# Optimization experiments

Measured on AMD Instinct MI355X. Metric: run time of the kernel, lower is better.

Reference implementation:

```python
import jax, jax.numpy as jnp
import numpy as np

B, S, E, H = 4, 1024, 1024, 16
D = E // H  # head_dim = 64


def setup_inputs() -> dict:
    key = jax.random.key(0)
    ks = jax.random.split(key, 12)
    s = 1.0 / np.sqrt(E)
    return {
        "query": jax.random.normal(ks[0], (B, S, E), jnp.float32),
        "key_": jax.random.normal(ks[1], (B, S, E), jnp.float32),
        "value": jax.random.normal(ks[2], (B, S, E), jnp.float32),
        "mask": jnp.ones((B, S, S), dtype=bool),
        "Wq": jax.random.uniform(ks[3], (E, E), jnp.float32, -s, s),
        "bq": jax.random.uniform(ks[4], (E,), jnp.float32, -s, s),
        "Wk": jax.random.uniform(ks[5], (E, E), jnp.float32, -s, s),
        "bk": jax.random.uniform(ks[6], (E,), jnp.float32, -s, s),
        "Wv": jax.random.uniform(ks[7], (E, E), jnp.float32, -s, s),
        "bv": jax.random.uniform(ks[8], (E,), jnp.float32, -s, s),
        "Wo": jax.random.uniform(ks[9], (E, E), jnp.float32, -s, s),
        "bo": jax.random.uniform(ks[10], (E,), jnp.float32, -s, s),
    }


def reference(query, key_, value, mask, Wq, bq, Wk, bk, Wv, bv, Wo, bo):
    # project and split heads: [B,S,E] -> [B,H,S,D]
    def heads(x, W, b):
        return (x @ W + b).reshape(B, -1, H, D).transpose(0, 2, 1, 3)

    q = heads(query, Wq, bq)
    k = heads(key_, Wk, bk)
    v = heads(value, Wv, bv)

    scores = jnp.einsum("bhqd,bhkd->bhqk", q, k) / jnp.sqrt(jnp.float32(D))
    # bool mask: positions where mask==0 are filled with -1e9
    scores = jnp.where(mask[:, None, :, :], scores, jnp.float32(-1e9))
    attn_weights = jax.nn.softmax(scores, axis=-1)  # [B,H,Sq,Sk]
    out = jnp.einsum("bhqk,bhkd->bhqd", attn_weights, v)
    out = out.transpose(0, 2, 1, 3).reshape(B, -1, E)  # [B,Sq,E]
    attn_output = out @ Wo + bo
    return attn_output, attn_weights
```

## Files before the change

kernel.cpp:

```cpp
#include <hip/hip_runtime.h>
#include <stdint.h>

typedef __bf16 bf16;
typedef bf16 bf16x2 __attribute__((ext_vector_type(2)));
typedef bf16 bf16x4 __attribute__((ext_vector_type(4)));
typedef bf16 bf16x8 __attribute__((ext_vector_type(8)));
typedef float f32x4 __attribute__((ext_vector_type(4)));
typedef float f32x16 __attribute__((ext_vector_type(16)));

static constexpr int Bc = 4, Sc = 1024, Ec = 1024, Hc = 16, Dc = 64, BSc = 4096;

__device__ __forceinline__ void gld_lds16(const void* g, void* s) {
  __builtin_amdgcn_global_load_lds((const __attribute__((address_space(1))) void*)g,
                                   (__attribute__((address_space(3))) void*)s, 16, 0, 0);
}

__global__ void detect_mask_kernel(const uint8_t* __restrict__ mask, int* flag) {
  if (threadIdx.x == 0 && blockIdx.x == 0) {
    bool everyGroupHasZero = true;
    bool anyNonzero = false;
    for (int j = 0; j < 16; ++j) {
      bool z = false;
      for (int bjj = 0; bjj < 4; ++bjj) {
        uint8_t byte = mask[4 * j + bjj];
        if (byte == 0) z = true;
        if (byte != 0) anyNonzero = true;
      }
      if (!z) everyGroupHasZero = false;
    }
    flag[0] = (everyGroupHasZero && anyNonzero) ? 4 : 1;
    flag[1] = 1;
  }
}

__global__ __launch_bounds__(256) void prep_kernel(
    const float* __restrict__ q, const float* __restrict__ k, const float* __restrict__ v,
    bf16* __restrict__ xb, const uint8_t* __restrict__ mask, int* __restrict__ mflag,
    const float* __restrict__ Wq, const float* __restrict__ Wk,
    const float* __restrict__ Wv, const float* __restrict__ Wo, bf16* __restrict__ wT) {
  __shared__ float tile[64][65];
  const int bid = blockIdx.x, t = threadIdx.x;

  if (bid < 2048) {
    const int n4 = (BSc * Ec) / 4;
    for (int i = bid * 256 + t; i < 3 * n4; i += 2048 * 256) {
      int which = i / n4;
      int off = i - which * n4;
      const float4* src = (which == 0) ? (const float4*)q : (which == 1) ? (const float4*)k : (const float4*)v;
      float4 f = src[off];
      bf16x4 o;
      o[0] = (bf16)f.x; o[1] = (bf16)f.y; o[2] = (bf16)f.z; o[3] = (bf16)f.w;
      *(bf16x4*)(xb + (size_t)which * BSc * Ec + (size_t)off * 4) = o;
    }
  } else if (bid < 3072) {
    bool everyGroupHasZero = true, anyNonzero = false;
    for (int j = 0; j < 16; ++j) {
      bool z = false;
      for (int bjj = 0; bjj < 4; ++bjj) {
        uint8_t byte = mask[4 * j + bjj];
        if (byte == 0) z = true;
        if (byte != 0) anyNonzero = true;
      }
      if (!z) everyGroupHasZero = false;
    }
    const int stride = (everyGroupHasZero && anyNonzero) ? 4 : 1;
    bool ok = true;
    const uint4* p = (const uint4*)mask;
    const int sb = bid - 2048;
    if (stride == 1) {
      const int n = (Bc * Sc * Sc) / 16;
      for (int i = sb * 256 + t; i < n; i += 1024 * 256) {
        uint4 w = p[i];
        uint32_t z = 0;
        z |= (w.x - 0x01010101u) & ~w.x;
        z |= (w.y - 0x01010101u) & ~w.y;
        z |= (w.z - 0x01010101u) & ~w.z;
        z |= (w.w - 0x01010101u) & ~w.w;
        if (z & 0x80808080u) ok = false;
      }
    } else {
      const int n = (Bc * Sc * Sc) / 4;
      for (int i = sb * 256 + t; i < n; i += 1024 * 256) {
        uint4 w = p[i];
        if (w.x == 0u || w.y == 0u || w.z == 0u || w.w == 0u) ok = false;
      }
    }
    if (!ok) atomicAnd(&mflag[1], 0);
  } else {
    const int i = bid - 3072;
    const int z = i >> 8, rem = i & 255;
    const int k0 = (rem & 15) * 64, n0 = (rem >> 4) * 64;
    const float* W = (z == 0) ? Wq : (z == 1) ? Wk : (z == 2) ? Wv : Wo;
    bf16* out = wT + (size_t)z * Ec * Ec;
#pragma unroll
    for (int p2 = 0; p2 < 16; p2++) {
      int r = p2 * 4 + (t >> 6), c = t & 63;
      tile[r][c] = W[(size_t)(k0 + r) * Ec + n0 + c];
    }
    __syncthreads();
#pragma unroll
    for (int p2 = 0; p2 < 8; p2++) {
      int n = p2 * 8 + (t >> 5), kk = (t & 31) * 2;
      bf16x2 v2;
      v2[0] = (bf16)tile[kk][n];
      v2[1] = (bf16)tile[kk + 1][n];
      *(bf16x2*)(out + (size_t)(n0 + n) * Ec + k0 + kk) = v2;
    }
  }
}

template <int MODE>
__global__ __launch_bounds__(256) void gemm128_kernel(
    const bf16* __restrict__ A_, const bf16* __restrict__ W_,
    const float* __restrict__ bias0, const float* __restrict__ bias1, const float* __restrict__ bias2,
    bf16* __restrict__ outb_, float* __restrict__ outf) {
  constexpr int K = 1024, N = 1024;
  const int z = blockIdx.z;
  const bf16* A = A_ + (size_t)z * BSc * K;
  const bf16* Wt = W_ + (size_t)z * N * K;
  const float* bias = (z == 0) ? bias0 : (z == 1) ? bias1 : bias2;
  bf16* outb = outb_ + (size_t)z * Bc * Hc * Sc * Dc;
  const float oscale = (MODE == 1 && z == 0) ? 0.125f : 1.0f;
  const int n0 = blockIdx.x * 128, m0 = blockIdx.y * 128;

  __shared__ bf16 As[128 * 64];
  __shared__ bf16 Bs[128 * 64];
  const int t = threadIdx.x, wave = t >> 6, lane = t & 63;
  const int wr = wave >> 1, wc = wave & 1;

  f32x4 acc[4][4];
#pragma unroll
  for (int i = 0; i < 4; i++)
#pragma unroll
    for (int j = 0; j < 4; j++)
#pragma unroll
      for (int r = 0; r < 4; r++) acc[i][j][r] = 0.f;

  const int srow = (lane >> 3);
  const int scol = (lane & 7) * 8;

  for (int kt = 0; kt < K; kt += 64) {
#pragma unroll
    for (int i = 0; i < 4; i++) {
      const int chunk = i * 4 + wave;
      const int row = chunk * 8 + srow;
      gld_lds16(A + (size_t)(m0 + row) * K + kt + scol, &As[chunk * 512]);
      gld_lds16(Wt + (size_t)(n0 + row) * K + kt + scol, &Bs[chunk * 512]);
    }
    __syncthreads();
#pragma unroll
    for (int kk = 0; kk < 2; kk++) {
      bf16x8 af[4], bg[4];
#pragma unroll
      for (int i = 0; i < 4; i++) {
        af[i] = *(const bf16x8*)&As[(64 * wr + i * 16 + (lane & 15)) * 64 + kk * 32 + (lane >> 4) * 8];
        bg[i] = *(const bf16x8*)&Bs[(64 * wc + i * 16 + (lane & 15)) * 64 + kk * 32 + (lane >> 4) * 8];
      }
#pragma unroll
      for (int mi = 0; mi < 4; mi++)
#pragma unroll
        for (int ni = 0; ni < 4; ni++)
          acc[mi][ni] = __builtin_amdgcn_mfma_f32_16x16x32_bf16(af[mi], bg[ni], acc[mi][ni], 0, 0, 0);
    }
    __syncthreads();
  }

#pragma unroll
  for (int mi = 0; mi < 4; mi++) {
#pragma unroll
    for (int ni = 0; ni < 4; ni++) {
      const int col = n0 + 64 * wc + ni * 16 + (lane & 15);
      const float bvl = bias[col];
#pragma unroll
      for (int r = 0; r < 4; r++) {
        const int row = m0 + 64 * wr + mi * 16 + (lane >> 4) * 4 + r;
        const float v = (acc[mi][ni][r] + bvl) * oscale;
        if (MODE == 0) {
          outf[(size_t)row * N + col] = v;
        } else {
          const int bidx = row >> 10, s = row & 1023, hh = col >> 6, d = col & 63;
          const int dst = (z == 1) ? (d ^ ((s & 7) << 3)) : d;
          outb[(((size_t)bidx * Hc + hh) * Sc + s) * Dc + dst] = (bf16)v;
        }
      }
    }
  }
}

__global__ __launch_bounds__(256) void transpose_v_kernel(const bf16* __restrict__ Vb,
                                                          bf16* __restrict__ VTb) {
  __shared__ bf16 tile[64][66];
  const int s0 = blockIdx.x * 64, bh = blockIdx.y;
  const bf16* src = Vb + (size_t)bh * Sc * Dc;
  bf16* dst = VTb + (size_t)bh * Dc * Sc;
  const int t = threadIdx.x;
#pragma unroll
  for (int p = 0; p < 8; p++) {
    int s = p * 8 + (t >> 5), d = (t & 31) * 2;
    *(bf16x2*)&tile[s][d] = *(const bf16x2*)(src + (size_t)(s0 + s) * Dc + d);
  }
  __syncthreads();
#pragma unroll
  for (int p = 0; p < 8; p++) {
    int d = p * 8 + (t >> 5), s = (t & 31) * 2;
    bf16x2 v2;
    v2[0] = tile[s][d];
    v2[1] = tile[s + 1][d];
    const int sidx = (s0 + s) ^ ((d & 7) << 3);
    *(bf16x2*)(dst + (size_t)d * Sc + sidx) = v2;
  }
}

__device__ __forceinline__ f32x16 qk_lds(const char* sK, const bf16x8 qf[4],
                                         int koff, int l31, int hi) {
  const int row = koff + l31;
  const char* base = sK + row * 128;
  const int sw = (row & 7) << 4;
  f32x16 a;
#pragma unroll
  for (int r = 0; r < 16; r++) a[r] = 0.f;
#pragma unroll
  for (int ks = 0; ks < 4; ks++) {
    const bf16x8 kf = *(const bf16x8*)(base + ((ks * 32 + hi * 16) ^ sw));
    a = __builtin_amdgcn_mfma_f32_32x32x16_bf16(kf, qf[ks], a, 0, 0, 0);
  }
  return a;
}

__device__ __forceinline__ void mask_app(f32x16& a, int kt, const uint8_t* mrow1,
                                         const uint8_t* mrow4, int mstride, int hi) {
  if (mstride == 1) {
#pragma unroll
    for (int gg = 0; gg < 4; gg++) {
      const int kg = kt + gg * 8 + hi * 4;
      const uint32_t mw = *(const uint32_t*)(mrow1 + kg);
#pragma unroll
      for (int r = 0; r < 4; r++)
        if (((mw >> (8 * r)) & 0xffu) == 0u) a[gg * 4 + r] = -1e9f;
    }
  } else {
#pragma unroll
    for (int gg = 0; gg < 4; gg++) {
      const int kg = kt + gg * 8 + hi * 4;
      const uint4 m4 = *(const uint4*)(mrow4 + (size_t)4 * kg);
      const uint32_t w[4] = {m4.x, m4.y, m4.z, m4.w};
#pragma unroll
      for (int r = 0; r < 4; r++)
        if (w[r] == 0u) a[gg * 4 + r] = -1e9f;
    }
  }
}

__global__ __launch_bounds__(256, 3) void attn_kernel(
    const bf16* __restrict__ Qb, const bf16* __restrict__ Kb, const bf16* __restrict__ VTb,
    const uint8_t* __restrict__ mask, const int* __restrict__ mflag,
    float* __restrict__ wout_, bf16* __restrict__ ctx) {
  const int qg = blockIdx.x, h = blockIdx.y, b = blockIdx.z;
  const int bh = b * Hc + h;
  const int t = threadIdx.x, wave = t >> 6, lane = t & 63;
  const int l31 = lane & 31, hi = lane >> 5;
  const int q0 = qg * 128 + wave * 32;
  const int q = q0 + l31;

  __shared__ __attribute__((aligned(16))) char smem[43008];
  bf16* Ptb = (bf16*)(smem + 32768) + wave * 1280;

  const bf16* Qp = Qb + ((size_t)bh * Sc + q) * Dc;
  bf16x8 qf[4];
#pragma unroll
  for (int ks = 0; ks < 4; ks++) qf[ks] = *(const bf16x8*)(Qp + ks * 16 + hi * 8);

  const int allTrue = mflag[1];
  const int mstride = mflag[0];
  const uint8_t* mrow1 = mask + (size_t)(b * Sc + q) * Sc;
  const uint8_t* mrow4 = mask + (size_t)(b * Sc + q) * Sc * 4;

  const char* Kbb = (const char*)(Kb + (size_t)bh * Sc * Dc);
  const char* VTbb = (const char*)(VTb + (size_t)bh * Dc * Sc);

  float m = -3.0e38f, l = 0.f;
#pragma unroll
  for (int j = 0; j < 2; j++) {
    const int off = j * 4096 + wave * 1024;
    gld_lds16(Kbb + off + lane * 16, smem + off);
  }
  __syncthreads();
  for (int st = 0; st < 16; st++) {
    const int cur = st & 1;
    if (st < 15) {
#pragma unroll
      for (int j = 0; j < 2; j++) {
        const int off = j * 4096 + wave * 1024;
        gld_lds16(Kbb + (st + 1) * 8192 + off + lane * 16, smem + (cur ^ 1) * 8192 + off);
      }
    }
    const char* sK = smem + cur * 8192;
#pragma unroll
    for (int tl = 0; tl < 2; tl++) {
      f32x16 a = qk_lds(sK, qf, tl * 32, l31, hi);
      if (!allTrue) mask_app(a, st * 64 + tl * 32, mrow1, mrow4, mstride, hi);
      float tm = a[0];
#pragma unroll
      for (int r = 1; r < 16; r++) tm = fmaxf(tm, a[r]);
      const float mnew = fmaxf(m, tm);
      float s = 0.f;
#pragma unroll
      for (int r = 0; r < 16; r++) s += __expf(a[r] - mnew);
      l = l * __expf(m - mnew) + s;
      m = mnew;
    }
    __syncthreads();
  }
  {
    const float mo = __shfl_xor(m, 32), lo = __shfl_xor(l, 32);
    const float M = fmaxf(m, mo);
    l = l * __expf(m - M) + lo * __expf(mo - M);
    m = M;
  }
  const float invl = 1.f / l;

  float* wbase = wout_ + ((size_t)bh * Sc + q0) * Sc;
  f32x16 oacc[2];
#pragma unroll
  for (int nj = 0; nj < 2; nj++)
#pragma unroll
    for (int r = 0; r < 16; r++) oacc[nj][r] = 0.f;

#pragma unroll
  for (int j = 0; j < 2; j++) {
    const int off = j * 4096 + wave * 1024;
    gld_lds16(Kbb + off + lane * 16, smem + off);
    const int goff = off + lane * 16;
    const int d = goff >> 7, ko = goff & 127;
    gld_lds16(VTbb + (size_t)d * 2048 + ko, smem + 16384 + off);
  }
  __syncthreads();
  for (int st = 0; st < 16; st++) {
    const int cur = st & 1;
    if (st < 15) {
#pragma unroll
      for (int j = 0; j < 2; j++) {
        const int off = j * 4096 + wave * 1024;
        gld_lds16(Kbb + (st + 1) * 8192 + off + lane * 16, smem + (cur ^ 1) * 8192 + off);
        const int goff = off + lane * 16;
        const int d = goff >> 7, ko = goff & 127;
        gld_lds16(VTbb + (size_t)d * 2048 + (st + 1) * 128 + ko,
                  smem + 16384 + (cur ^ 1) * 8192 + off);
      }
    }
    const char* sK = smem + cur * 8192;
    const char* sV = smem + 16384 + cur * 8192;
#pragma unroll
    for (int tl = 0; tl < 2; tl++) {
      f32x16 a = qk_lds(sK, qf, tl * 32, l31, hi);
      if (!allTrue) mask_app(a, st * 64 + tl * 32, mrow1, mrow4, mstride, hi);
#pragma unroll
      for (int gg = 0; gg < 4; gg++) {
        bf16x4 p4;
#pragma unroll
        for (int r = 0; r < 4; r++) p4[r] = (bf16)(__expf(a[gg * 4 + r] - m) * invl);
        *(bf16x4*)&Ptb[l31 * 40 + gg * 8 + hi * 4] = p4;
      }
#pragma unroll
      for (int i = 0; i < 4; i++) {
        const int q2 = 8 * i + (lane >> 3), kk = (lane & 7) * 4;
        const bf16x4 pv4 = *(const bf16x4*)&Ptb[q2 * 40 + kk];
        f32x4 v4;
#pragma unroll
        for (int r = 0; r < 4; r++) v4[r] = (float)pv4[r];
        __builtin_nontemporal_store(v4,
            (f32x4*)(wbase + (size_t)q2 * Sc + st * 64 + tl * 32 + kk));
      }
#pragma unroll
      for (int stq = 0; stq < 2; stq++) {
        const bf16x8 pa = *(const bf16x8*)&Ptb[l31 * 40 + stq * 16 + hi * 8];
#pragma unroll
        for (int nj = 0; nj < 2; nj++) {
          const int d = nj * 32 + l31;
          const int off = ((tl * 32 + stq * 16 + hi * 8) * 2) ^ ((d & 7) << 4);
          const bf16x8 bv = *(const bf16x8*)(sV + d * 128 + off);
          oacc[nj] = __builtin_amdgcn_mfma_f32_32x32x16_bf16(pa, bv, oacc[nj], 0, 0, 0);
        }
      }
    }
    __syncthreads();
  }

#pragma unroll
  for (int nj = 0; nj < 2; nj++) {
#pragma unroll
    for (int rg = 0; rg < 16; rg++) {
      const int qq = (rg & 3) + 8 * (rg >> 2) + 4 * hi;
      Ptb[qq * 40 + l31] = (bf16)oacc[nj][rg];
    }
    const int rr = lane >> 1, c0 = (lane & 1) * 16;
    const bf16x8 o0 = *(const bf16x8*)&Ptb[rr * 40 + c0];
    const bf16x8 o1 = *(const bf16x8*)&Ptb[rr * 40 + c0 + 8];
    bf16* cbase = ctx + ((size_t)(b * Sc + q0 + rr)) * Ec + h * Dc + nj * 32 + c0;
    *(bf16x8*)cbase = o0;
    *(bf16x8*)(cbase + 8) = o1;
  }
}

extern "C" void kernel_launch(void* const* d_in, const int* in_sizes, int n_in,
                              void* d_out, int out_size, void* d_ws, size_t ws_size,
                              hipStream_t stream) {
  const float* q = (const float*)d_in[0];
  const float* k = (const float*)d_in[1];
  const float* v = (const float*)d_in[2];
  const uint8_t* mask = (const uint8_t*)d_in[3];
  const float* Wq = (const float*)d_in[4];
  const float* bq = (const float*)d_in[5];
  const float* Wk = (const float*)d_in[6];
  const float* bk = (const float*)d_in[7];
  const float* Wv = (const float*)d_in[8];
  const float* bv = (const float*)d_in[9];
  const float* Wo = (const float*)d_in[10];
  const float* bo = (const float*)d_in[11];

  bf16* wsb = (bf16*)d_ws;
  bf16* xb = wsb;
  bf16* ctx = wsb;
  bf16* VTb = wsb + (size_t)4 * 1024 * 1024;
  bf16* wT = wsb + (size_t)12 * 1024 * 1024;
  bf16* Qb = wsb + (size_t)16 * 1024 * 1024;
  bf16* Kb = wsb + (size_t)20 * 1024 * 1024;
  bf16* Vb = wsb + (size_t)24 * 1024 * 1024;
  int* mflag = (int*)((char*)d_ws + (size_t)56 * 1024 * 1024);

  float* outf = (float*)d_out;
  float* attnw = outf + (size_t)4 * 1024 * 1024;

  detect_mask_kernel<<<1, 64, 0, stream>>>(mask, mflag);
  prep_kernel<<<4096, 256, 0, stream>>>(q, k, v, xb, mask, mflag, Wq, Wk, Wv, Wo, wT);
  gemm128_kernel<1><<<dim3(8, 32, 3), 256, 0, stream>>>(xb, wT, bq, bk, bv, Qb, nullptr);
  transpose_v_kernel<<<dim3(16, 64), 256, 0, stream>>>(Vb, VTb);
  attn_kernel<<<dim3(8, 16, 4), 256, 0, stream>>>(Qb, Kb, VTb, mask, mflag, attnw, ctx);
  gemm128_kernel<0><<<dim3(8, 32, 1), 256, 0, stream>>>(ctx, wT + (size_t)3 * 1024 * 1024,
                                                        bo, bo, bo, nullptr, outf);
}
```

Measured before the change: 188.1 us.

## Fuse V transpose into projection GEMM epilogue and drop mask-detect kernel

The V projection GEMM now writes its output already transposed and XOR-swizzled into VTb, staging it through shared memory in the epilogue, so the separate transpose_v_kernel and its extra global round trip go away. The single-thread detect_mask_kernel is replaced by a memset plus flag writes inside prep_kernel, with the flag layout changed to an OR-based 'not all true' bit. This removes two launches and one intermediate buffer pass, in exchange for a more complex GEMM epilogue and extra barriers in the z==2 blocks.

```diff
diff --git a/kernel.cpp b/kernel.cpp
--- a/kernel.cpp
+++ b/kernel.cpp
@@ -13,24 +13,6 @@
 __device__ __forceinline__ void gld_lds16(const void* g, void* s) {
   __builtin_amdgcn_global_load_lds((const __attribute__((address_space(1))) void*)g,
                                    (__attribute__((address_space(3))) void*)s, 16, 0, 0);
-}
-
-__global__ void detect_mask_kernel(const uint8_t* __restrict__ mask, int* flag) {
-  if (threadIdx.x == 0 && blockIdx.x == 0) {
-    bool everyGroupHasZero = true;
-    bool anyNonzero = false;
-    for (int j = 0; j < 16; ++j) {
-      bool z = false;
-      for (int bjj = 0; bjj < 4; ++bjj) {
-        uint8_t byte = mask[4 * j + bjj];
-        if (byte == 0) z = true;
-        if (byte != 0) anyNonzero = true;
-      }
-      if (!z) everyGroupHasZero = false;
-    }
-    flag[0] = (everyGroupHasZero && anyNonzero) ? 4 : 1;
-    flag[1] = 1;
-  }
 }
 
 __global__ __launch_bounds__(256) void prep_kernel(
@@ -64,6 +46,7 @@
       if (!z) everyGroupHasZero = false;
     }
     const int stride = (everyGroupHasZero && anyNonzero) ? 4 : 1;
+    if (t == 0) mflag[1] = stride;
     bool ok = true;
     const uint4* p = (const uint4*)mask;
     const int sb = bid - 2048;
@@ -85,7 +68,7 @@
         if (w.x == 0u || w.y == 0u || w.z == 0u || w.w == 0u) ok = false;
       }
     }
-    if (!ok) atomicAnd(&mflag[1], 0);
+    if (!ok) atomicOr(&mflag[0], 1);
   } else {
     const int i = bid - 3072;
     const int z = i >> 8, rem = i & 255;
@@ -113,7 +96,7 @@
 __global__ __launch_bounds__(256) void gemm128_kernel(
     const bf16* __restrict__ A_, const bf16* __restrict__ W_,
     const float* __restrict__ bias0, const float* __restrict__ bias1, const float* __restrict__ bias2,
-    bf16* __restrict__ outb_, float* __restrict__ outf) {
+    bf16* __restrict__ outb_, float* __restrict__ outf, bf16* __restrict__ VTb) {
   constexpr int K = 1024, N = 1024;
   const int z = blockIdx.z;
   const bf16* A = A_ + (size_t)z * BSc * K;
@@ -123,8 +106,9 @@
   const float oscale = (MODE == 1 && z == 0) ? 0.125f : 1.0f;
   const int n0 = blockIdx.x * 128, m0 = blockIdx.y * 128;
 
-  __shared__ bf16 As[128 * 64];
-  __shared__ bf16 Bs[128 * 64];
+  __shared__ __attribute__((aligned(16))) char gsm[32768];
+  bf16* As = (bf16*)gsm;
+  bf16* Bs = (bf16*)(gsm + 16384);
   const int t = threadIdx.x, wave = t >> 6, lane = t & 63;
   const int wr = wave >> 1, wc = wave & 1;
 
@@ -163,6 +147,45 @@
           acc[mi][ni] = __builtin_amdgcn_mfma_f32_16x16x32_bf16(af[mi], bg[ni], acc[mi][ni], 0, 0, 0);
     }
     __syncthreads();
+  }
+
+  if (MODE == 1 && z == 2) {
+    bf16* vtw = (bf16*)gsm + wave * 2304;
+    const int head = (n0 >> 6) + wc;
+    const int bidx = (m0 + 64 * wr) >> 10;
+    const int sbase = (m0 + 64 * wr) & 1023;
+    bf16* vbase = VTb + ((size_t)(bidx * Hc + head) * Dc) * Sc;
+#pragma unroll
+    for (int h2 = 0; h2 < 2; h2++) {
+      __syncthreads();
+#pragma unroll
+      for (int mi = 0; mi < 4; mi++) {
+#pragma unroll
+        for (int ni2 = 0; ni2 < 2; ni2++) {
+          const int ni = h2 * 2 + ni2;
+          const float bvl = bias[n0 + 64 * wc + ni * 16 + (lane & 15)];
+          const int dl = ni2 * 16 + (lane & 15);
+#pragma unroll
+          for (int rp = 0; rp < 2; rp++) {
+            bf16x2 v2;
+            v2[0] = (bf16)(acc[mi][ni][rp * 2] + bvl);
+            v2[1] = (bf16)(acc[mi][ni][rp * 2 + 1] + bvl);
+            *(bf16x2*)&vtw[dl * 72 + mi * 16 + (lane >> 4) * 4 + rp * 2] = v2;
+          }
+        }
+      }
+      __syncthreads();
+#pragma unroll
+      for (int i2 = 0; i2 < 4; i2++) {
+        const int dl = i2 * 8 + (lane >> 3);
+        const int d = h2 * 32 + dl;
+        const int cp = lane & 7;
+        const int cs = cp ^ (d & 7);
+        const bf16x8 vv = *(const bf16x8*)&vtw[dl * 72 + cs * 8];
+        *(bf16x8*)(vbase + (size_t)d * Sc + sbase + cp * 8) = vv;
+      }
+    }
+    return;
   }
 
 #pragma unroll
@@ -187,30 +210,6 @@
   }
 }
 
-__global__ __launch_bounds__(256) void transpose_v_kernel(const bf16* __restrict__ Vb,
-                                                          bf16* __restrict__ VTb) {
-  __shared__ bf16 tile[64][66];
-  const int s0 = blockIdx.x * 64, bh = blockIdx.y;
-  const bf16* src = Vb + (size_t)bh * Sc * Dc;
-  bf16* dst = VTb + (size_t)bh * Dc * Sc;
-  const int t = threadIdx.x;
-#pragma unroll
-  for (int p = 0; p < 8; p++) {
-    int s = p * 8 + (t >> 5), d = (t & 31) * 2;
-    *(bf16x2*)&tile[s][d] = *(const bf16x2*)(src + (size_t)(s0 + s) * Dc + d);
-  }
-  __syncthreads();
-#pragma unroll
-  for (int p = 0; p < 8; p++) {
-    int d = p * 8 + (t >> 5), s = (t & 31) * 2;
-    bf16x2 v2;
-    v2[0] = tile[s][d];
-    v2[1] = tile[s + 1][d];
-    const int sidx = (s0 + s) ^ ((d & 7) << 3);
-    *(bf16x2*)(dst + (size_t)d * Sc + sidx) = v2;
-  }
-}
-
 __device__ __forceinline__ f32x16 qk_lds(const char* sK, const bf16x8 qf[4],
                                          int koff, int l31, int hi) {
   const int row = koff + l31;
@@ -270,8 +269,8 @@
 #pragma unroll
   for (int ks = 0; ks < 4; ks++) qf[ks] = *(const bf16x8*)(Qp + ks * 16 + hi * 8);
 
-  const int allTrue = mflag[1];
-  const int mstride = mflag[0];
+  const int allTrue = !mflag[0];
+  const int mstride = mflag[1];
   const uint8_t* mrow1 = mask + (size_t)(b * Sc + q) * Sc;
   const uint8_t* mrow4 = mask + (size_t)(b * Sc + q) * Sc * 4;
 
@@ -421,21 +420,19 @@
   bf16* wsb = (bf16*)d_ws;
   bf16* xb = wsb;
   bf16* ctx = wsb;
-  bf16* VTb = wsb + (size_t)4 * 1024 * 1024;
   bf16* wT = wsb + (size_t)12 * 1024 * 1024;
   bf16* Qb = wsb + (size_t)16 * 1024 * 1024;
   bf16* Kb = wsb + (size_t)20 * 1024 * 1024;
-  bf16* Vb = wsb + (size_t)24 * 1024 * 1024;
+  bf16* VTb = wsb + (size_t)24 * 1024 * 1024;
   int* mflag = (int*)((char*)d_ws + (size_t)56 * 1024 * 1024);
 
   float* outf = (float*)d_out;
   float* attnw = outf + (size_t)4 * 1024 * 1024;
 
-  detect_mask_kernel<<<1, 64, 0, stream>>>(mask, mflag);
+  hipMemsetAsync(mflag, 0, 8, stream);
   prep_kernel<<<4096, 256, 0, stream>>>(q, k, v, xb, mask, mflag, Wq, Wk, Wv, Wo, wT);
-  gemm128_kernel<1><<<dim3(8, 32, 3), 256, 0, stream>>>(xb, wT, bq, bk, bv, Qb, nullptr);
-  transpose_v_kernel<<<dim3(16, 64), 256, 0, stream>>>(Vb, VTb);
+  gemm128_kernel<1><<<dim3(8, 32, 3), 256, 0, stream>>>(xb, wT, bq, bk, bv, Qb, nullptr, VTb);
   attn_kernel<<<dim3(8, 16, 4), 256, 0, stream>>>(Qb, Kb, VTb, mask, mflag, attnw, ctx);
   gemm128_kernel<0><<<dim3(8, 32, 1), 256, 0, stream>>>(ctx, wT + (size_t)3 * 1024 * 1024,
-                                                        bo, bo, bo, nullptr, outf);
-}
+                                                        bo, bo, bo, nullptr, outf, nullptr);
+}
```

After: 185.1 us. No clear change (-1.6%).
